# Optimization experiments

Hardware: AMD Instinct MI355X
Metric: run time of the kernel (lower is better)

The kernel has to match this reference:

```python
import jax, jax.numpy as jnp
import numpy as np

KSIZE = 3   # patch kernel
NSIZE = 7   # search neighborhood
SCALE = 4   # downscale factor
ALPHA = 1


def _patches(x, k, pad_mode):
    # x: [b,c,h,w] -> [b, c*k*k, h, w], feature ordering channel-major
    # (matches torch.nn.functional.unfold ordering).
    if pad_mode == 'reflect':
        p = k // 2
        xp = jnp.pad(x, ((0, 0), (0, 0), (p, p), (p, p)), mode='reflect')
        return jax.lax.conv_general_dilated_patches(xp, (k, k), (1, 1), 'VALID')
    return jax.lax.conv_general_dilated_patches(x, (k, k), (1, 1), 'SAME')


def census(x):
    # UFlow-style soft census transform (the CensusTransform used in this repo):
    # grayscale*255, 3x3 zero-padded patches minus center, soft-sign normalize.
    gray = (0.299 * x[:, 0:1] + 0.587 * x[:, 1:2] + 0.114 * x[:, 2:3]) * 255.0
    p = _patches(gray, KSIZE, 'zero')          # [b, 9, h, w]
    t = p - gray
    return t / jnp.sqrt(0.81 + t * t)


def downsample(x):
    b, c, h, w = x.shape
    return jax.image.resize(x, (b, c, h // SCALE, w // SCALE), method='cubic')


def unfold_center(x):
    # _unfold(data, with_unfold=False): [b,c,h,w] -> [b, hw, c*k*k]
    x = downsample(x)
    b, c, h, w = x.shape
    p = _patches(x, KSIZE, 'reflect').reshape(b, c * KSIZE * KSIZE, h * w)
    return p.transpose(0, 2, 1)


def unfold_nbr(x):
    # _unfold(data, with_unfold=True): [b,c,h,w] -> [b, hw, n*n, c*k*k]
    x = downsample(x)
    b, c, h, w = x.shape
    d1 = _patches(x, KSIZE, 'reflect')          # [b, c*k*k, h, w]
    c1 = d1.shape[1]
    d2 = _patches(d1, NSIZE, 'reflect')         # [b, c1*n*n, h, w]
    d2 = d2.reshape(b, c1, NSIZE * NSIZE, h * w)
    return d2.transpose(0, 3, 2, 1)


def reference(pred, I):
    # --- census-space distance + argmin over 2*n*n candidates ---
    p_ct = unfold_center(census(pred))                       # [b, hw, 81]
    nbr_ct = jnp.concatenate(
        [unfold_nbr(census(I[:, 0])), unfold_nbr(census(I[:, 1]))], axis=2
    )                                                        # [b, hw, 2n^2, 81]
    # ||p - n||^2 expanded as p2 + n2 - 2 p.n (avoids the huge repeated diff)
    p2 = jnp.sum(p_ct * p_ct, axis=-1)                       # [b, hw]
    n2 = jnp.sum(nbr_ct * nbr_ct, axis=-1)                   # [b, hw, 2n^2]
    dis = p2[:, :, None] + n2 - 2.0 * jnp.einsum('bpc,bpnc->bpn', p_ct, nbr_ct)
    ind = jnp.argmin(dis, axis=2)                            # [b, hw]
    # --- gather matched raw patches and compute loss ---
    p = unfold_center(pred)                                  # [b, hw, 27]
    nbr = jnp.concatenate(
        [unfold_nbr(I[:, 0]), unfold_nbr(I[:, 1])], axis=2
    )                                                        # [b, hw, 2n^2, 27]
    matched = jnp.take_along_axis(nbr, ind[:, :, None, None], axis=2)[:, :, 0]
    return jnp.mean((p - matched) ** 2 * 0.5)


def setup_inputs() -> dict:
    key = jax.random.key(0)
    k1, k2 = jax.random.split(key)
    pred = jax.random.normal(k1, (2, 3, 384, 384), dtype=jnp.float32)
    I = jax.random.normal(k2, (2, 2, 3, 384, 384), dtype=jnp.float32)
    return {'pred': pred, 'I': I}
```

## Files before the change

### kernel.cpp

```cpp
#include <hip/hip_runtime.h>
#include <math.h>

#define FH 384
#define FW 384
#define DH 96
#define DW 96
#define NIMG 6
#define PLANE (DH * DW)
#define NPIX (2 * PLANE)

__device__ __forceinline__ float keysc(float x) {
    if (x < 1.f) return ((1.5f * x - 2.5f) * x) * x + 1.f;
    if (x < 2.f) return ((-0.5f * x + 2.5f) * x - 4.f) * x + 2.f;
    return 0.f;
}

__device__ __forceinline__ int refl(int i, int n) {
    if (i < 0) i = -i;
    if (i >= n) i = 2 * (n - 1) - i;
    return i;
}

__global__ void k_field(const float* __restrict__ pred, const float* __restrict__ I,
                        float* __restrict__ CF) {
    int idx = blockIdx.x * 256 + threadIdx.x;
    const int total = NIMG * FH * FW;
    if (idx >= total) return;
    int x   = idx % FW;
    int t1  = idx / FW;
    int r   = t1 % FH;
    int img = t1 / FH;
    const float* src;
    if (img < 2) {
        src = pred + img * 3 * FH * FW;
    } else {
        int j = (img - 2) >> 1, b = (img - 2) & 1;
        src = I + ((b * 2 + j) * 3) * FH * FW;
    }
    const int planeF = FH * FW;
    auto grayAt = [&](int rr, int cc) -> float {
        const float* s = src + rr * FW + cc;
        return (0.299f * s[0] + 0.587f * s[planeF] + 0.114f * s[2 * planeF]) * 255.0f;
    };
    float gc = grayAt(r, x);
    float* out = CF + ((size_t)img * 8) * planeF + r * FW + x;
    int ck = 0;
#pragma unroll
    for (int k = 0; k < 9; ++k) {
        if (k == 4) continue;
        int dy = k / 3 - 1, dx = k % 3 - 1;
        int r2 = r + dy, c2 = x + dx;
        float gn = (r2 < 0 || r2 >= FH || c2 < 0 || c2 >= FW) ? 0.f : grayAt(r2, c2);
        float tt = gn - gc;
        out[ck * planeF] = tt / sqrtf(0.81f + tt * tt);
        ++ck;
    }
}

#define CQ (NIMG * 9 * (DH / 4) * (FW / 4))
#define RQ (NIMG * 3 * (DH / 4) * (FW / 4))
__global__ void k_downH(const float* __restrict__ CF, const float* __restrict__ pred,
                        const float* __restrict__ I, float* __restrict__ CH,
                        float* __restrict__ RH) {
    int idx = blockIdx.x * 256 + threadIdx.x;
    if (idx >= CQ + RQ) return;
    const int planeF = FH * FW;

    const float4* F;
    float4* outp;
    int yo0;
    if (idx < CQ) {
        int x4 = idx % 96;
        int t1 = idx / 96;
        int ys = t1 % (DH / 4);
        int t2 = t1 / (DH / 4);
        int k  = t2 % 9;
        int img = t2 / 9;
        yo0 = ys * 4;
        outp = (float4*)CH + ((img * 9 + k) * DH + yo0) * 96 + x4;
        if (k == 4) {
            float4 zz = make_float4(0.f, 0.f, 0.f, 0.f);
#pragma unroll
            for (int q = 0; q < 4; ++q) outp[q * 96] = zz;
            return;
        }
        int ck = (k < 4) ? k : k - 1;
        F = (const float4*)(CF + (size_t)(img * 8 + ck) * planeF) + x4;
    } else {
        int rid = idx - CQ;
        int x4 = rid % 96;
        int t1 = rid / 96;
        int ys = t1 % (DH / 4);
        int t2 = t1 / (DH / 4);
        int c  = t2 % 3;
        int img = t2 / 3;
        yo0 = ys * 4;
        const float* src;
        if (img < 2) {
            src = pred + (img * 3 + c) * planeF;
        } else {
            int j = (img - 2) >> 1, b = (img - 2) & 1;
            src = I + (((b * 2 + j) * 3) + c) * planeF;
        }
        F = (const float4*)src + x4;
        outp = (float4*)RH + ((img * 3 + c) * DH + yo0) * 96 + x4;
    }

    int rbase0 = 4 * yo0 - 6;
    float4 acc0 = make_float4(0.f, 0.f, 0.f, 0.f), acc1 = acc0, acc2 = acc0, acc3 = acc0;
    float z0 = 0.f, z1 = 0.f, z2 = 0.f, z3 = 0.f;
#pragma unroll
    for (int rr = 0; rr < 28; ++rr) {
        int ra = rbase0 + rr;
        bool valid = (ra >= 0 && ra < FH);
        float4 v = make_float4(0.f, 0.f, 0.f, 0.f);
        if (valid) v = F[ra * 96];
        { int t = rr;      if (t < 16 && valid)            { float w = keysc(fabsf((float)t - 7.5f) * 0.25f); z0 += w; acc0.x += w * v.x; acc0.y += w * v.y; acc0.z += w * v.z; acc0.w += w * v.w; } }
        { int t = rr - 4;  if (t >= 0 && t < 16 && valid)  { float w = keysc(fabsf((float)t - 7.5f) * 0.25f); z1 += w; acc1.x += w * v.x; acc1.y += w * v.y; acc1.z += w * v.z; acc1.w += w * v.w; } }
        { int t = rr - 8;  if (t >= 0 && t < 16 && valid)  { float w = keysc(fabsf((float)t - 7.5f) * 0.25f); z2 += w; acc2.x += w * v.x; acc2.y += w * v.y; acc2.z += w * v.z; acc2.w += w * v.w; } }
        { int t = rr - 12; if (t >= 0 && t < 16 && valid)  { float w = keysc(fabsf((float)t - 7.5f) * 0.25f); z3 += w; acc3.x += w * v.x; acc3.y += w * v.y; acc3.z += w * v.z; acc3.w += w * v.w; } }
    }
    outp[0]      = make_float4(acc0.x / z0, acc0.y / z0, acc0.z / z0, acc0.w / z0);
    outp[96]     = make_float4(acc1.x / z1, acc1.y / z1, acc1.z / z1, acc1.w / z1);
    outp[2 * 96] = make_float4(acc2.x / z2, acc2.y / z2, acc2.z / z2, acc2.w / z2);
    outp[3 * 96] = make_float4(acc3.x / z3, acc3.y / z3, acc3.z / z3, acc3.w / z3);
}

__global__ void k_downW(const float* __restrict__ src, float* __restrict__ dst, int nrows) {
    int idx = blockIdx.x * 256 + threadIdx.x;
    int total = nrows * DW;
    if (idx >= total) return;
    int xo = idx % DW;
    int row = idx / DW;
    const float* s = src + row * FW;
    float acc = 0.f, z = 0.f;
#pragma unroll
    for (int t = 0; t < 16; ++t) {
        int i = 4 * xo - 6 + t;
        if (i < 0 || i >= FW) continue;
        float w = keysc(fabsf((float)t - 7.5f) * 0.25f);
        z += w;
        acc += w * s[i];
    }
    dst[idx] = acc / z;
}

__global__ void k_n2(const float* __restrict__ CD, float* __restrict__ N2,
                     int* __restrict__ counter) {
    int idx = blockIdx.x * 256 + threadIdx.x;
    if (idx == 0) *counter = 0;
    if (idx >= 4 * PLANE) return;
    int img4 = idx / PLANE;
    int pos  = idx % PLANE;
    int y = pos / DW, x = pos % DW;
    int ry[3], rx[3];
#pragma unroll
    for (int kk = 0; kk < 3; ++kk) {
        ry[kk] = refl(y + kk - 1, DH);
        rx[kk] = refl(x + kk - 1, DW);
    }
    const float* C = CD + (2 + img4) * 9 * PLANE;
    float s = 0.f;
#pragma unroll
    for (int c = 0; c < 9; ++c)
#pragma unroll
        for (int ky = 0; ky < 3; ++ky)
#pragma unroll
            for (int kx = 0; kx < 3; ++kx) {
                float v = C[c * PLANE + ry[ky] * DW + rx[kx]];
                s += v * v;
            }
    N2[idx] = s;
}

__global__ __launch_bounds__(256) void k_match_int(const float* __restrict__ CD,
                                                   const float* __restrict__ N2,
                                                   float* __restrict__ bestd,
                                                   int* __restrict__ bestn) {
    int bid  = blockIdx.x;
    int g    = bid / 72;
    int tile = bid % 72;
    int pid  = tile * 256 + threadIdx.x;
    int j  = g / 7;
    int dy = g % 7 - 3;
    int b   = pid / PLANE;
    int pos = pid % PLANE;
    int y = pos / DW, x = pos % DW;

    int yy = refl(y + dy, DH);
    int r0 = refl(yy - 1, DH), r1 = yy, r2 = refl(yy + 1, DH);
    int pr0 = refl(y - 1, DH), pr2 = refl(y + 1, DH);
    int xb = min(max(x - 4, 0), DW - 9);
    int xp = min(max(x - 1, 0), DW - 3);

    const float* Cp  = CD + (b * 9) * PLANE;
    const float* Cn  = CD + ((2 + 2 * j + b) * 9) * PLANE;
    const float* N2p = N2 + (2 * j + b) * PLANE;

    float dot[7];
#pragma unroll
    for (int i = 0; i < 7; ++i) dot[i] = 0.f;

#pragma unroll
    for (int c = 0; c < 9; ++c) {
        const float* pc = Cp + c * PLANE;
        const float* nc = Cn + c * PLANE;
        float p0[3], p1[3], p2[3];
#pragma unroll
        for (int kx = 0; kx < 3; ++kx) {
            p0[kx] = pc[pr0 * DW + xp + kx];
            p1[kx] = pc[y   * DW + xp + kx];
            p2[kx] = pc[pr2 * DW + xp + kx];
        }
        float w0[9], w1[9], w2[9];
#pragma unroll
        for (int i = 0; i < 9; ++i) {
            w0[i] = nc[r0 * DW + xb + i];
            w1[i] = nc[r1 * DW + xb + i];
            w2[i] = nc[r2 * DW + xb + i];
        }
#pragma unroll
        for (int dx = 0; dx < 7; ++dx) {
            float d = dot[dx];
            d += p0[0] * w0[dx + 0]; d += p0[1] * w0[dx + 1]; d += p0[2] * w0[dx + 2];
            d += p1[0] * w1[dx + 0]; d += p1[1] * w1[dx + 1]; d += p1[2] * w1[dx + 2];
            d += p2[0] * w2[dx + 0]; d += p2[1] * w2[dx + 1]; d += p2[2] * w2[dx + 2];
            dot[dx] = d;
        }
    }

    float best = INFINITY;
    int bn = 1 << 30;
    int nbase = j * 49 + (dy + 3) * 7;
#pragma unroll
    for (int dx = 0; dx < 7; ++dx) {
        int xxc = min(max(x + dx - 3, 0), DW - 1);
        float dis = N2p[yy * DW + xxc] - 2.f * dot[dx];
        if (dis < best) { best = dis; bn = nbase + dx; }
    }
    if (x >= 4 && x < 92) {
        bestd[g * NPIX + pid] = best;
        bestn[g * NPIX + pid] = bn;
    }
}

__global__ __launch_bounds__(256) void k_match_edge(const float* __restrict__ CD,
                                                    const float* __restrict__ N2,
                                                    float* __restrict__ bestd,
                                                    int* __restrict__ bestn) {
    __shared__ float part[4][64];
    __shared__ float disw[4][8];

    int wid  = threadIdx.x >> 6;
    int lane = threadIdx.x & 63;
    int item = blockIdx.x * 4 + wid;
    int g  = item / 1536;
    int pe = item % 1536;
    int j = g / 7, dy = g % 7 - 3;
    int b   = pe / 768;
    int rem = pe % 768;
    int y  = rem / 8;
    int xi = rem % 8;
    int x  = (xi < 4) ? xi : 88 + xi;
    int pid = b * PLANE + y * DW + x;
    int yy = refl(y + dy, DH);

    int c = lane / 7, dx = lane % 7;
    float partial = 0.f;
    if (lane < 63) {
        int xx = refl(x + dx - 3, DW);
        const float* pc = CD + (b * 9 + c) * PLANE;
        const float* nc = CD + ((2 + 2 * j + b) * 9 + c) * PLANE;
#pragma unroll
        for (int ky = 0; ky < 3; ++ky) {
            int pry = refl(y + ky - 1, DH);
            int nry = refl(yy + ky - 1, DH);
#pragma unroll
            for (int kx = 0; kx < 3; ++kx) {
                int prx = refl(x + kx - 1, DW);
                int nrx = refl(xx + kx - 1, DW);
                partial += pc[pry * DW + prx] * nc[nry * DW + nrx];
            }
        }
    }
    part[wid][lane] = partial;
    __syncthreads();

    if (lane < 7) {
        float dot = 0.f;
#pragma unroll
        for (int cc = 0; cc < 9; ++cc) dot += part[wid][cc * 7 + lane];
        int xxl = refl(x + lane - 3, DW);
        disw[wid][lane] = N2[(2 * j + b) * PLANE + yy * DW + xxl] - 2.f * dot;
    }
    __syncthreads();

    if (lane == 0) {
        float best = INFINITY;
        int bn = 1 << 30;
        int nbase = j * 49 + (dy + 3) * 7;
#pragma unroll
        for (int dxx = 0; dxx < 7; ++dxx) {
            float d = disw[wid][dxx];
            if (d < best) { best = d; bn = nbase + dxx; }
        }
        bestd[g * NPIX + pid] = best;
        bestn[g * NPIX + pid] = bn;
    }
}

#define NPART 72
__global__ __launch_bounds__(256) void k_combine(const float* __restrict__ bestd,
                                                 const int* __restrict__ bestn,
                                                 const float* __restrict__ RD,
                                                 float* __restrict__ partial,
                                                 int* __restrict__ counter,
                                                 float* __restrict__ out) {
    int pid = blockIdx.x * 256 + threadIdx.x;
    int b   = pid / PLANE;
    int pos = pid % PLANE;
    int y = pos / DW, x = pos % DW;

    float d0 = bestd[pid];
    int   n0 = bestn[pid];
#pragma unroll
    for (int g = 1; g < 14; ++g) {
        float d = bestd[g * NPIX + pid];
        int   n = bestn[g * NPIX + pid];
        if (d < d0 || (d == d0 && n < n0)) { d0 = d; n0 = n; }
    }

    int j = n0 / 49, rr = n0 % 49;
    int dy = rr / 7 - 3, dx = rr % 7 - 3;
    int yy = refl(y + dy, DH), xx = refl(x + dx, DW);
    int ry0[3], rx0[3], ry[3], rx[3];
#pragma unroll
    for (int kk = 0; kk < 3; ++kk) {
        ry0[kk] = refl(y + kk - 1, DH);
        rx0[kk] = refl(x + kk - 1, DW);
        ry[kk]  = refl(yy + kk - 1, DH);
        rx[kk]  = refl(xx + kk - 1, DW);
    }
    const float* RDp = RD + b * 3 * PLANE;
    const float* RDn = RD + (2 + 2 * j + b) * 3 * PLANE;
    float loss = 0.f;
#pragma unroll
    for (int c = 0; c < 3; ++c)
#pragma unroll
        for (int ky = 0; ky < 3; ++ky)
#pragma unroll
            for (int kx = 0; kx < 3; ++kx) {
                float a = RDp[c * PLANE + ry0[ky] * DW + rx0[kx]];
                float m = RDn[c * PLANE + ry[ky] * DW + rx[kx]];
                float d = a - m;
                loss += d * d;
            }

    __shared__ float red[256];
    __shared__ int sdone;
    red[threadIdx.x] = loss;
    __syncthreads();
#pragma unroll
    for (int s = 128; s > 0; s >>= 1) {
        if (threadIdx.x < s) red[threadIdx.x] += red[threadIdx.x + s];
        __syncthreads();
    }
    if (threadIdx.x == 0) {
        __hip_atomic_store(&partial[blockIdx.x], red[0], __ATOMIC_RELEASE,
                           __HIP_MEMORY_SCOPE_AGENT);
        int prev = __hip_atomic_fetch_add(counter, 1, __ATOMIC_ACQ_REL,
                                          __HIP_MEMORY_SCOPE_AGENT);
        sdone = (prev == NPART - 1);
    }
    __syncthreads();

    if (sdone) {
        __shared__ float red2[128];
        if (threadIdx.x < 128) {
            float v = (threadIdx.x < NPART)
                ? __hip_atomic_load(&partial[threadIdx.x], __ATOMIC_ACQUIRE,
                                    __HIP_MEMORY_SCOPE_AGENT)
                : 0.f;
            red2[threadIdx.x] = v;
        }
        __syncthreads();
#pragma unroll
        for (int s = 64; s > 0; s >>= 1) {
            if (threadIdx.x < s) red2[threadIdx.x] += red2[threadIdx.x + s];
            __syncthreads();
        }
        if (threadIdx.x == 0) out[0] = red2[0] * (0.5f / 497664.0f);
    }
}

extern "C" void kernel_launch(void* const* d_in, const int* in_sizes, int n_in,
                              void* d_out, int out_size, void* d_ws, size_t ws_size,
                              hipStream_t stream) {
    const float* pred = (const float*)d_in[0];
    const float* I    = (const float*)d_in[1];
    float* out = (float*)d_out;
    float* ws  = (float*)d_ws;

    float* CD   = ws;
    float* RD   = CD + 497664;
    float* S    = RD + 165888;
    float* CF   = S;
    float* CH   = S + 7077888;
    float* RH   = S + 9068544;
    float* N2   = S;
    float* bestd = S + 36864;
    int*   bestn = (int*)(S + 294912);
    float* part  = S + 552960;
    int*   counter = (int*)(S + 553032);

    k_field<<<(NIMG * FH * FW + 255) / 256, 256, 0, stream>>>(pred, I, CF);
    k_downH<<<(CQ + RQ + 255) / 256, 256, 0, stream>>>(CF, pred, I, CH, RH);
    k_downW<<<((NIMG * 12 * DH) * DW + 255) / 256, 256, 0, stream>>>(CH, CD, NIMG * 12 * DH);
    k_n2<<<(4 * PLANE + 255) / 256, 256, 0, stream>>>(CD, N2, counter);
    k_match_int<<<14 * 72, 256, 0, stream>>>(CD, N2, bestd, bestn);
    k_match_edge<<<(14 * 1536) / 4, 256, 0, stream>>>(CD, N2, bestd, bestn);
    k_combine<<<NPIX / 256, 256, 0, stream>>>(bestd, bestn, RD, part, counter, out);
}
```

Before: 118.6 us.

## Fuse census computation into vertical downsample and split match over dx halves

The full-resolution 8-channel census field is no longer stored. A small kernel writes grayscale, and the vertical cubic downsample computes the soft-sign census differences on the fly from neighbouring gray values. This cuts a large intermediate write and read in exchange for repeated softsign work per tap. Separately, the interior match kernel splits each dy group into two dx halves (4 and 3 candidates), doubling the grid to 28 groups for more parallelism and fewer registers. The edge kernel and the combine step are adjusted for the new slot layout.

Result: slower. 139.6 us (+17.7%).

```diff
diff --git a/kernel.cpp b/kernel.cpp
--- a/kernel.cpp
+++ b/kernel.cpp
@@ -21,15 +21,17 @@
     return i;
 }
 
-__global__ void k_field(const float* __restrict__ pred, const float* __restrict__ I,
-                        float* __restrict__ CF) {
+__device__ __forceinline__ float softsign(float t) {
+    return t / sqrtf(0.81f + t * t);
+}
+
+__global__ void k_gray(const float* __restrict__ pred, const float* __restrict__ I,
+                       float* __restrict__ gray) {
     int idx = blockIdx.x * 256 + threadIdx.x;
     const int total = NIMG * FH * FW;
     if (idx >= total) return;
-    int x   = idx % FW;
-    int t1  = idx / FW;
-    int r   = t1 % FH;
-    int img = t1 / FH;
+    int img = idx / (FH * FW);
+    int px  = idx % (FH * FW);
     const float* src;
     if (img < 2) {
         src = pred + img * 3 * FH * FW;
@@ -37,38 +39,19 @@
         int j = (img - 2) >> 1, b = (img - 2) & 1;
         src = I + ((b * 2 + j) * 3) * FH * FW;
     }
-    const int planeF = FH * FW;
-    auto grayAt = [&](int rr, int cc) -> float {
-        const float* s = src + rr * FW + cc;
-        return (0.299f * s[0] + 0.587f * s[planeF] + 0.114f * s[2 * planeF]) * 255.0f;
-    };
-    float gc = grayAt(r, x);
-    float* out = CF + ((size_t)img * 8) * planeF + r * FW + x;
-    int ck = 0;
-#pragma unroll
-    for (int k = 0; k < 9; ++k) {
-        if (k == 4) continue;
-        int dy = k / 3 - 1, dx = k % 3 - 1;
-        int r2 = r + dy, c2 = x + dx;
-        float gn = (r2 < 0 || r2 >= FH || c2 < 0 || c2 >= FW) ? 0.f : grayAt(r2, c2);
-        float tt = gn - gc;
-        out[ck * planeF] = tt / sqrtf(0.81f + tt * tt);
-        ++ck;
-    }
+    float r = src[px], g = src[FH * FW + px], b = src[2 * FH * FW + px];
+    gray[idx] = (0.299f * r + 0.587f * g + 0.114f * b) * 255.0f;
 }
 
 #define CQ (NIMG * 9 * (DH / 4) * (FW / 4))
 #define RQ (NIMG * 3 * (DH / 4) * (FW / 4))
-__global__ void k_downH(const float* __restrict__ CF, const float* __restrict__ pred,
+__global__ void k_downH(const float* __restrict__ gray, const float* __restrict__ pred,
                         const float* __restrict__ I, float* __restrict__ CH,
                         float* __restrict__ RH) {
     int idx = blockIdx.x * 256 + threadIdx.x;
     if (idx >= CQ + RQ) return;
     const int planeF = FH * FW;
 
-    const float4* F;
-    float4* outp;
-    int yo0;
     if (idx < CQ) {
         int x4 = idx % 96;
         int t1 = idx / 96;
@@ -76,16 +59,58 @@
         int t2 = t1 / (DH / 4);
         int k  = t2 % 9;
         int img = t2 / 9;
-        yo0 = ys * 4;
-        outp = (float4*)CH + ((img * 9 + k) * DH + yo0) * 96 + x4;
+        int yo0 = ys * 4;
+        float4* outp = (float4*)CH + ((img * 9 + k) * DH + yo0) * 96 + x4;
         if (k == 4) {
             float4 zz = make_float4(0.f, 0.f, 0.f, 0.f);
 #pragma unroll
             for (int q = 0; q < 4; ++q) outp[q * 96] = zz;
             return;
         }
-        int ck = (k < 4) ? k : k - 1;
-        F = (const float4*)(CF + (size_t)(img * 8 + ck) * planeF) + x4;
+        int dy = k / 3 - 1, dx = k % 3 - 1;
+        const float* g = gray + img * planeF;
+        int xb = 4 * x4;
+
+        int rbase0 = 4 * yo0 - 6;
+        float4 acc0 = make_float4(0.f, 0.f, 0.f, 0.f), acc1 = acc0, acc2 = acc0, acc3 = acc0;
+        float z0 = 0.f, z1 = 0.f, z2 = 0.f, z3 = 0.f;
+#pragma unroll
+        for (int rr = 0; rr < 28; ++rr) {
+            int ra = rbase0 + rr;
+            if (ra < 0 || ra >= FH) continue;
+            const float* rowc = g + ra * FW + xb;
+            float4 gc = *(const float4*)rowc;
+            int r2 = ra + dy;
+            float4 gn;
+            if (r2 < 0 || r2 >= FH) {
+                gn = make_float4(0.f, 0.f, 0.f, 0.f);
+            } else {
+                const float* rown = g + r2 * FW + xb;
+                if (dx == 0) {
+                    gn = *(const float4*)rown;
+                } else if (dx == -1) {
+                    float4 A = *(const float4*)rown;
+                    float pw = (xb > 0) ? rown[-1] : 0.f;
+                    gn = make_float4(pw, A.x, A.y, A.z);
+                } else {
+                    float4 A = *(const float4*)rown;
+                    float nx = (xb + 4 < FW) ? rown[4] : 0.f;
+                    gn = make_float4(A.y, A.z, A.w, nx);
+                }
+            }
+            float s0 = softsign(gn.x - gc.x);
+            float s1 = softsign(gn.y - gc.y);
+            float s2 = softsign(gn.z - gc.z);
+            float s3 = softsign(gn.w - gc.w);
+            { int t = rr;      if (t < 16)           { float w = keysc(fabsf((float)t - 7.5f) * 0.25f); z0 += w; acc0.x += w * s0; acc0.y += w * s1; acc0.z += w * s2; acc0.w += w * s3; } }
+            { int t = rr - 4;  if (t >= 0 && t < 16) { float w = keysc(fabsf((float)t - 7.5f) * 0.25f); z1 += w; acc1.x += w * s0; acc1.y += w * s1; acc1.z += w * s2; acc1.w += w * s3; } }
+            { int t = rr - 8;  if (t >= 0 && t < 16) { float w = keysc(fabsf((float)t - 7.5f) * 0.25f); z2 += w; acc2.x += w * s0; acc2.y += w * s1; acc2.z += w * s2; acc2.w += w * s3; } }
+            { int t = rr - 12; if (t >= 0 && t < 16) { float w = keysc(fabsf((float)t - 7.5f) * 0.25f); z3 += w; acc3.x += w * s0; acc3.y += w * s1; acc3.z += w * s2; acc3.w += w * s3; } }
+        }
+        outp[0]      = make_float4(acc0.x / z0, acc0.y / z0, acc0.z / z0, acc0.w / z0);
+        outp[96]     = make_float4(acc1.x / z1, acc1.y / z1, acc1.z / z1, acc1.w / z1);
+        outp[2 * 96] = make_float4(acc2.x / z2, acc2.y / z2, acc2.z / z2, acc2.w / z2);
+        outp[3 * 96] = make_float4(acc3.x / z3, acc3.y / z3, acc3.z / z3, acc3.w / z3);
     } else {
         int rid = idx - CQ;
         int x4 = rid % 96;
@@ -94,7 +119,7 @@
         int t2 = t1 / (DH / 4);
         int c  = t2 % 3;
         int img = t2 / 3;
-        yo0 = ys * 4;
+        int yo0 = ys * 4;
         const float* src;
         if (img < 2) {
             src = pred + (img * 3 + c) * planeF;
@@ -102,28 +127,27 @@
             int j = (img - 2) >> 1, b = (img - 2) & 1;
             src = I + (((b * 2 + j) * 3) + c) * planeF;
         }
-        F = (const float4*)src + x4;
-        outp = (float4*)RH + ((img * 3 + c) * DH + yo0) * 96 + x4;
-    }
-
-    int rbase0 = 4 * yo0 - 6;
-    float4 acc0 = make_float4(0.f, 0.f, 0.f, 0.f), acc1 = acc0, acc2 = acc0, acc3 = acc0;
-    float z0 = 0.f, z1 = 0.f, z2 = 0.f, z3 = 0.f;
-#pragma unroll
-    for (int rr = 0; rr < 28; ++rr) {
-        int ra = rbase0 + rr;
-        bool valid = (ra >= 0 && ra < FH);
-        float4 v = make_float4(0.f, 0.f, 0.f, 0.f);
-        if (valid) v = F[ra * 96];
-        { int t = rr;      if (t < 16 && valid)            { float w = keysc(fabsf((float)t - 7.5f) * 0.25f); z0 += w; acc0.x += w * v.x; acc0.y += w * v.y; acc0.z += w * v.z; acc0.w += w * v.w; } }
-        { int t = rr - 4;  if (t >= 0 && t < 16 && valid)  { float w = keysc(fabsf((float)t - 7.5f) * 0.25f); z1 += w; acc1.x += w * v.x; acc1.y += w * v.y; acc1.z += w * v.z; acc1.w += w * v.w; } }
-        { int t = rr - 8;  if (t >= 0 && t < 16 && valid)  { float w = keysc(fabsf((float)t - 7.5f) * 0.25f); z2 += w; acc2.x += w * v.x; acc2.y += w * v.y; acc2.z += w * v.z; acc2.w += w * v.w; } }
-        { int t = rr - 12; if (t >= 0 && t < 16 && valid)  { float w = keysc(fabsf((float)t - 7.5f) * 0.25f); z3 += w; acc3.x += w * v.x; acc3.y += w * v.y; acc3.z += w * v.z; acc3.w += w * v.w; } }
-    }
-    outp[0]      = make_float4(acc0.x / z0, acc0.y / z0, acc0.z / z0, acc0.w / z0);
-    outp[96]     = make_float4(acc1.x / z1, acc1.y / z1, acc1.z / z1, acc1.w / z1);
-    outp[2 * 96] = make_float4(acc2.x / z2, acc2.y / z2, acc2.z / z2, acc2.w / z2);
-    outp[3 * 96] = make_float4(acc3.x / z3, acc3.y / z3, acc3.z / z3, acc3.w / z3);
+        const float4* F = (const float4*)src + x4;
+        float4* outp = (float4*)RH + ((img * 3 + c) * DH + yo0) * 96 + x4;
+
+        int rbase0 = 4 * yo0 - 6;
+        float4 acc0 = make_float4(0.f, 0.f, 0.f, 0.f), acc1 = acc0, acc2 = acc0, acc3 = acc0;
+        float z0 = 0.f, z1 = 0.f, z2 = 0.f, z3 = 0.f;
+#pragma unroll
+        for (int rr = 0; rr < 28; ++rr) {
+            int ra = rbase0 + rr;
+            if (ra < 0 || ra >= FH) continue;
+            float4 v = F[ra * 96];
+            { int t = rr;      if (t < 16)           { float w = keysc(fabsf((float)t - 7.5f) * 0.25f); z0 += w; acc0.x += w * v.x; acc0.y += w * v.y; acc0.z += w * v.z; acc0.w += w * v.w; } }
+            { int t = rr - 4;  if (t >= 0 && t < 16) { float w = keysc(fabsf((float)t - 7.5f) * 0.25f); z1 += w; acc1.x += w * v.x; acc1.y += w * v.y; acc1.z += w * v.z; acc1.w += w * v.w; } }
+            { int t = rr - 8;  if (t >= 0 && t < 16) { float w = keysc(fabsf((float)t - 7.5f) * 0.25f); z2 += w; acc2.x += w * v.x; acc2.y += w * v.y; acc2.z += w * v.z; acc2.w += w * v.w; } }
+            { int t = rr - 12; if (t >= 0 && t < 16) { float w = keysc(fabsf((float)t - 7.5f) * 0.25f); z3 += w; acc3.x += w * v.x; acc3.y += w * v.y; acc3.z += w * v.z; acc3.w += w * v.w; } }
+        }
+        outp[0]      = make_float4(acc0.x / z0, acc0.y / z0, acc0.z / z0, acc0.w / z0);
+        outp[96]     = make_float4(acc1.x / z1, acc1.y / z1, acc1.z / z1, acc1.w / z1);
+        outp[2 * 96] = make_float4(acc2.x / z2, acc2.y / z2, acc2.z / z2, acc2.w / z2);
+        outp[3 * 96] = make_float4(acc3.x / z3, acc3.y / z3, acc3.z / z3, acc3.w / z3);
+    }
 }
 
 __global__ void k_downW(const float* __restrict__ src, float* __restrict__ dst, int nrows) {
@@ -173,6 +197,7 @@
     N2[idx] = s;
 }
 
+#define NGRP 28
 __global__ __launch_bounds__(256) void k_match_int(const float* __restrict__ CD,
                                                    const float* __restrict__ N2,
                                                    float* __restrict__ bestd,
@@ -181,8 +206,11 @@
     int g    = bid / 72;
     int tile = bid % 72;
     int pid  = tile * 256 + threadIdx.x;
-    int j  = g / 7;
-    int dy = g % 7 - 3;
+    int j   = g / 14;
+    int r14 = g % 14;
+    int dyi = r14 >> 1;
+    int h   = r14 & 1;
+    int dy  = dyi - 3;
     int b   = pid / PLANE;
     int pos = pid % PLANE;
     int y = pos / DW, x = pos % DW;
@@ -196,48 +224,88 @@
     const float* Cp  = CD + (b * 9) * PLANE;
     const float* Cn  = CD + ((2 + 2 * j + b) * 9) * PLANE;
     const float* N2p = N2 + (2 * j + b) * PLANE;
-
-    float dot[7];
-#pragma unroll
-    for (int i = 0; i < 7; ++i) dot[i] = 0.f;
-
-#pragma unroll
-    for (int c = 0; c < 9; ++c) {
-        const float* pc = Cp + c * PLANE;
-        const float* nc = Cn + c * PLANE;
-        float p0[3], p1[3], p2[3];
-#pragma unroll
-        for (int kx = 0; kx < 3; ++kx) {
-            p0[kx] = pc[pr0 * DW + xp + kx];
-            p1[kx] = pc[y   * DW + xp + kx];
-            p2[kx] = pc[pr2 * DW + xp + kx];
-        }
-        float w0[9], w1[9], w2[9];
-#pragma unroll
-        for (int i = 0; i < 9; ++i) {
-            w0[i] = nc[r0 * DW + xb + i];
-            w1[i] = nc[r1 * DW + xb + i];
-            w2[i] = nc[r2 * DW + xb + i];
-        }
-#pragma unroll
-        for (int dx = 0; dx < 7; ++dx) {
-            float d = dot[dx];
-            d += p0[0] * w0[dx + 0]; d += p0[1] * w0[dx + 1]; d += p0[2] * w0[dx + 2];
-            d += p1[0] * w1[dx + 0]; d += p1[1] * w1[dx + 1]; d += p1[2] * w1[dx + 2];
-            d += p2[0] * w2[dx + 0]; d += p2[1] * w2[dx + 1]; d += p2[2] * w2[dx + 2];
-            dot[dx] = d;
-        }
-    }
+    int nbase = j * 49 + dyi * 7;
 
     float best = INFINITY;
     int bn = 1 << 30;
-    int nbase = j * 49 + (dy + 3) * 7;
-#pragma unroll
-    for (int dx = 0; dx < 7; ++dx) {
-        int xxc = min(max(x + dx - 3, 0), DW - 1);
-        float dis = N2p[yy * DW + xxc] - 2.f * dot[dx];
-        if (dis < best) { best = dis; bn = nbase + dx; }
-    }
+
+    if (h == 0) {
+        float dot[4];
+#pragma unroll
+        for (int i = 0; i < 4; ++i) dot[i] = 0.f;
+#pragma unroll
+        for (int c = 0; c < 9; ++c) {
+            const float* pc = Cp + c * PLANE;
+            const float* nc = Cn + c * PLANE;
+            float p0[3], p1[3], p2[3];
+#pragma unroll
+            for (int kx = 0; kx < 3; ++kx) {
+                p0[kx] = pc[pr0 * DW + xp + kx];
+                p1[kx] = pc[y   * DW + xp + kx];
+                p2[kx] = pc[pr2 * DW + xp + kx];
+            }
+            float w0[6], w1[6], w2[6];
+#pragma unroll
+            for (int i = 0; i < 6; ++i) {
+                w0[i] = nc[r0 * DW + xb + i];
+                w1[i] = nc[r1 * DW + xb + i];
+                w2[i] = nc[r2 * DW + xb + i];
+            }
+#pragma unroll
+            for (int a = 0; a < 4; ++a) {
+                float d = dot[a];
+                d += p0[0] * w0[a + 0]; d += p0[1] * w0[a + 1]; d += p0[2] * w0[a + 2];
+                d += p1[0] * w1[a + 0]; d += p1[1] * w1[a + 1]; d += p1[2] * w1[a + 2];
+                d += p2[0] * w2[a + 0]; d += p2[1] * w2[a + 1]; d += p2[2] * w2[a + 2];
+                dot[a] = d;
+            }
+        }
+#pragma unroll
+        for (int a = 0; a < 4; ++a) {
+            int xxc = min(max(x + a - 3, 0), DW - 1);
+            float dis = N2p[yy * DW + xxc] - 2.f * dot[a];
+            if (dis < best) { best = dis; bn = nbase + a; }
+        }
+    } else {
+        float dot[3];
+#pragma unroll
+        for (int i = 0; i < 3; ++i) dot[i] = 0.f;
+#pragma unroll
+        for (int c = 0; c < 9; ++c) {
+            const float* pc = Cp + c * PLANE;
+            const float* nc = Cn + c * PLANE;
+            float p0[3], p1[3], p2[3];
+#pragma unroll
+            for (int kx = 0; kx < 3; ++kx) {
+                p0[kx] = pc[pr0 * DW + xp + kx];
+                p1[kx] = pc[y   * DW + xp + kx];
+                p2[kx] = pc[pr2 * DW + xp + kx];
+            }
+            float w0[5], w1[5], w2[5];
+#pragma unroll
+            for (int i = 0; i < 5; ++i) {
+                w0[i] = nc[r0 * DW + xb + 4 + i];
+                w1[i] = nc[r1 * DW + xb + 4 + i];
+                w2[i] = nc[r2 * DW + xb + 4 + i];
+            }
+#pragma unroll
+            for (int a = 0; a < 3; ++a) {
+                float d = dot[a];
+                d += p0[0] * w0[a + 0]; d += p0[1] * w0[a + 1]; d += p0[2] * w0[a + 2];
+                d += p1[0] * w1[a + 0]; d += p1[1] * w1[a + 1]; d += p1[2] * w1[a + 2];
+                d += p2[0] * w2[a + 0]; d += p2[1] * w2[a + 1]; d += p2[2] * w2[a + 2];
+                dot[a] = d;
+            }
+        }
+#pragma unroll
+        for (int a = 0; a < 3; ++a) {
+            int dxa = a + 4;
+            int xxc = min(max(x + dxa - 3, 0), DW - 1);
+            float dis = N2p[yy * DW + xxc] - 2.f * dot[a];
+            if (dis < best) { best = dis; bn = nbase + dxa; }
+        }
+    }
+
     if (x >= 4 && x < 92) {
         bestd[g * NPIX + pid] = best;
         bestn[g * NPIX + pid] = bn;
@@ -254,9 +322,9 @@
     int wid  = threadIdx.x >> 6;
     int lane = threadIdx.x & 63;
     int item = blockIdx.x * 4 + wid;
-    int g  = item / 1536;
-    int pe = item % 1536;
-    int j = g / 7, dy = g % 7 - 3;
+    int g14 = item / 1536;
+    int pe  = item % 1536;
+    int j = g14 / 7, dyi = g14 % 7, dy = dyi - 3;
     int b   = pe / 768;
     int rem = pe % 768;
     int y  = rem / 8;
@@ -298,14 +366,17 @@
     if (lane == 0) {
         float best = INFINITY;
         int bn = 1 << 30;
-        int nbase = j * 49 + (dy + 3) * 7;
+        int nbase = j * 49 + dyi * 7;
 #pragma unroll
         for (int dxx = 0; dxx < 7; ++dxx) {
             float d = disw[wid][dxx];
             if (d < best) { best = d; bn = nbase + dxx; }
         }
-        bestd[g * NPIX + pid] = best;
-        bestn[g * NPIX + pid] = bn;
+        int s0 = j * 14 + dyi * 2;
+        bestd[s0 * NPIX + pid] = best;
+        bestn[s0 * NPIX + pid] = bn;
+        bestd[(s0 + 1) * NPIX + pid] = INFINITY;
+        bestn[(s0 + 1) * NPIX + pid] = 1 << 30;
     }
 }
 
@@ -324,7 +395,7 @@
     float d0 = bestd[pid];
     int   n0 = bestn[pid];
 #pragma unroll
-    for (int g = 1; g < 14; ++g) {
+    for (int g = 1; g < NGRP; ++g) {
         float d = bestd[g * NPIX + pid];
         int   n = bestn[g * NPIX + pid];
         if (d < d0 || (d == d0 && n < n0)) { d0 = d; n0 = n; }
@@ -404,20 +475,20 @@
     float* CD   = ws;
     float* RD   = CD + 497664;
     float* S    = RD + 165888;
-    float* CF   = S;
-    float* CH   = S + 7077888;
-    float* RH   = S + 9068544;
+    float* gray = S;
+    float* CH   = S + 884736;
+    float* RH   = S + 2875392;
     float* N2   = S;
     float* bestd = S + 36864;
-    int*   bestn = (int*)(S + 294912);
-    float* part  = S + 552960;
-    int*   counter = (int*)(S + 553032);
-
-    k_field<<<(NIMG * FH * FW + 255) / 256, 256, 0, stream>>>(pred, I, CF);
-    k_downH<<<(CQ + RQ + 255) / 256, 256, 0, stream>>>(CF, pred, I, CH, RH);
+    int*   bestn = (int*)(S + 1069056);
+    float* part  = S + 2101248;
+    int*   counter = (int*)(S + 2101320);
+
+    k_gray<<<(NIMG * FH * FW + 255) / 256, 256, 0, stream>>>(pred, I, gray);
+    k_downH<<<(CQ + RQ + 255) / 256, 256, 0, stream>>>(gray, pred, I, CH, RH);
     k_downW<<<((NIMG * 12 * DH) * DW + 255) / 256, 256, 0, stream>>>(CH, CD, NIMG * 12 * DH);
     k_n2<<<(4 * PLANE + 255) / 256, 256, 0, stream>>>(CD, N2, counter);
-    k_match_int<<<14 * 72, 256, 0, stream>>>(CD, N2, bestd, bestn);
+    k_match_int<<<NGRP * 72, 256, 0, stream>>>(CD, N2, bestd, bestn);
     k_match_edge<<<(14 * 1536) / 4, 256, 0, stream>>>(CD, N2, bestd, bestn);
     k_combine<<<NPIX / 256, 256, 0, stream>>>(bestd, bestn, RD, part, counter, out);
 }
```
